# Kernel tuning notes

Hardware: AMD Instinct MI355X
Metric: run time of the kernel (lower is better)

Reference implementation:

```python
import jax, jax.numpy as jnp
import numpy as np

N = 50000   # nodes per modality sub-graph
M = 20000   # hyperedges per modality
E = 200000  # incidences per modality
D = 128     # kg_emb_dim
H = 8       # mha_n_heads
C = 64      # context entities
NE = 200000 # n_entity


def hyper_conv(x, theta, bias, node_idx, edge_idx, num_edges):
    """PyG HypergraphConv (no attention): out = D^-1 H B^-1 H^T (X Theta) + b."""
    xt = x @ theta                                   # [N, D]
    n = x.shape[0]
    ones = jnp.ones(node_idx.shape, dtype=xt.dtype)
    B = jax.ops.segment_sum(ones, edge_idx, num_segments=num_edges)   # edge degree [M]
    Dn = jax.ops.segment_sum(ones, node_idx, num_segments=n)          # node degree [N]
    Binv = jnp.where(B > 0, 1.0 / B, 0.0)
    Dinv = jnp.where(Dn > 0, 1.0 / Dn, 0.0)
    e = jax.ops.segment_sum(xt[node_idx], edge_idx, num_segments=num_edges) * Binv[:, None]
    out = jax.ops.segment_sum(e[edge_idx], node_idx, num_segments=n) * Dinv[:, None]
    return out + bias


def mha(q_in, kv, wq, bq, wk, bk, wv, bv, wo, bo, n_heads):
    """torch.nn.MultiheadAttention(batch_first) with batch=1: query=[C,D], kv=[R,D]."""
    c, d = q_in.shape
    r = kv.shape[0]
    hd = d // n_heads
    q = (q_in @ wq + bq).reshape(c, n_heads, hd).transpose(1, 0, 2)   # [H,C,hd]
    k = (kv @ wk + bk).reshape(r, n_heads, hd).transpose(1, 0, 2)     # [H,R,hd]
    v = (kv @ wv + bv).reshape(r, n_heads, hd).transpose(1, 0, 2)     # [H,R,hd]
    scores = jnp.einsum('hcd,hrd->hcr', q, k) / jnp.sqrt(jnp.asarray(hd, q.dtype))
    attn = jax.nn.softmax(scores, axis=-1)
    o = jnp.einsum('hcr,hrd->hcd', attn, v)                           # [H,C,hd]
    o = o.transpose(1, 0, 2).reshape(c, d)
    return o @ wo + bo


def setup_inputs() -> dict:
    key = jax.random.key(0)
    ks = jax.random.split(key, 24)
    s = D ** -0.5
    inp = {
        'x_item': jax.random.normal(ks[0], (N, D), jnp.float32) * s,
        'theta_item': jax.random.normal(ks[1], (D, D), jnp.float32) * s,
        'bias_item': jnp.zeros((D,), jnp.float32),
        'x_ent': jax.random.normal(ks[2], (N, D), jnp.float32) * s,
        'theta_ent': jax.random.normal(ks[3], (D, D), jnp.float32) * s,
        'bias_ent': jnp.zeros((D,), jnp.float32),
        'x_word': jax.random.normal(ks[4], (N, D), jnp.float32) * s,
        'theta_word': jax.random.normal(ks[5], (D, D), jnp.float32) * s,
        'bias_word': jnp.zeros((D,), jnp.float32),
        'context': jax.random.normal(ks[6], (C, D), jnp.float32),
        'wq': jax.random.normal(ks[7], (D, D), jnp.float32) * s,
        'bq': jnp.zeros((D,), jnp.float32),
        'wk': jax.random.normal(ks[8], (D, D), jnp.float32) * s,
        'bk': jnp.zeros((D,), jnp.float32),
        'wv': jax.random.normal(ks[9], (D, D), jnp.float32) * s,
        'bv': jnp.zeros((D,), jnp.float32),
        'wo': jax.random.normal(ks[10], (D, D), jnp.float32) * s,
        'bo': jnp.zeros((D,), jnp.float32),
        'w_rec': jax.random.normal(ks[11], (D, NE), jnp.float32) * s,
        'b_rec': jnp.zeros((NE,), jnp.float32),
        'node_item': jax.random.randint(ks[12], (E,), 0, N, jnp.int32),
        'edge_item': jax.random.randint(ks[13], (E,), 0, M, jnp.int32),
        'node_ent': jax.random.randint(ks[14], (E,), 0, N, jnp.int32),
        'edge_ent': jax.random.randint(ks[15], (E,), 0, M, jnp.int32),
        'node_word': jax.random.randint(ks[16], (E,), 0, N, jnp.int32),
        'edge_word': jax.random.randint(ks[17], (E,), 0, M, jnp.int32),
        'num_edges': M,
    }
    return inp


def reference(x_item, theta_item, bias_item, x_ent, theta_ent, bias_ent,
              x_word, theta_word, bias_word, context,
              wq, bq, wk, bk, wv, bv, wo, bo, w_rec, b_rec,
              node_item, edge_item, node_ent, edge_ent, node_word, edge_word,
              num_edges):
    # Hypergraph conv per modality (item / entity / word sub-graphs)
    item_emb = hyper_conv(x_item, theta_item, bias_item, node_item, edge_item, num_edges)
    ent_emb = hyper_conv(x_ent, theta_ent, bias_ent, node_ent, edge_ent, num_edges)
    word_emb = hyper_conv(x_word, theta_word, bias_word, node_word, edge_word, num_edges)
    # related = cat(session_embedding, knowledge_embedding) across modalities
    related = jnp.concatenate([item_emb, ent_emb, word_emb], axis=0)   # [3N, D]
    # MHItemAttention: MHA(context, related, related)
    attentive = mha(context, related, wq, bq, wk, bk, wv, bv, wo, bo, H)  # [C, D]
    # Mean pooling path of _attention_and_gating
    user_repr = jnp.mean(attentive, axis=0)                            # [D]
    user_repr = jnp.mean(jnp.concatenate([context, user_repr[None]], axis=0), axis=0)
    # rec_bias: Linear(kg_emb_dim, n_entity)
    scores = user_repr @ w_rec + b_rec                                 # [n_entity]
    return scores
```

## Files before the change

### kernel.cpp

```cpp
#include <hip/hip_runtime.h>
#include <hip/hip_bf16.h>

constexpr int N_NODES = 50000;
constexpr int M_EDGES = 20000;
constexpr int E_INC   = 200000;
constexpr int H_HEADS = 8;
constexpr int C_CTX   = 64;
constexpr int NE_OUT  = 200000;
constexpr int R_REL   = 3 * N_NODES;

constexpr int STRIPS  = 128;
constexpr int SROWS   = 1172;

constexpr int NSL   = 64;
constexpr int SE    = (M_EDGES + NSL - 1) / NSL;
constexpr int SN    = (N_NODES + NSL - 1) / NSL;
constexpr int CAP_E = 40;
constexpr int CAP_N = 24;

typedef short bf8v __attribute__((ext_vector_type(8)));
typedef float f4v  __attribute__((ext_vector_type(4)));
#define MFMA16(a, b, c) __builtin_amdgcn_mfma_f32_16x16x32_bf16(a, b, c, 0, 0, 0)

__device__ __forceinline__ unsigned short bfs(float f) {
    union { __hip_bfloat16 b; unsigned short s; } u;
    u.b = __float2bfloat16(f);
    return u.s;
}
__device__ __forceinline__ unsigned bfp(float lo, float hi) {
    union { __hip_bfloat162 b; unsigned u; } v;
    v.b = __float22bfloat162_rn(make_float2(lo, hi));
    return v.u;
}

__device__ __forceinline__ void gload16(const void* g, const void* l) {
    __builtin_amdgcn_global_load_lds(
        (const __attribute__((address_space(1))) void*)(unsigned long long)(size_t)g,
        (__attribute__((address_space(3))) void*)(unsigned)(size_t)l,
        16, 0, 0);
}

__global__ __launch_bounds__(256) void zero_kernel(float4* p, int n4) {
    int i = blockIdx.x * 256 + threadIdx.x;
    if (i < n4) p[i] = make_float4(0.f, 0.f, 0.f, 0.f);
}

__global__ __launch_bounds__(256) void wconv_kernel(
    const float* __restrict__ t0, const float* __restrict__ t1,
    const float* __restrict__ t2, unsigned short* __restrict__ out)
{
    int idx = blockIdx.x * 256 + threadIdx.x;
    int m = idx >> 14, p = idx & 16383;
    int n = p >> 7, k = p & 127;
    const float* src = (m == 0) ? t0 : (m == 1) ? t1 : t2;
    out[idx] = bfs(src[k * 128 + n]);
}

__global__ __launch_bounds__(256) void qkf_kernel(
    const float* __restrict__ ctx, const float* __restrict__ wq,
    const float* __restrict__ bq, const float* __restrict__ wk,
    const float* __restrict__ bk, unsigned short* __restrict__ qkb,
    float* __restrict__ cb)
{
    __shared__ float qrow[128];
    const int c = blockIdx.x, t = threadIdx.x;
    if (t < 128) {
        float s = bq[t];
        for (int k = 0; k < 128; ++k) s += ctx[c * 128 + k] * wq[(size_t)k * 128 + t];
        qrow[t] = s;
    }
    __syncthreads();
#pragma unroll
    for (int i = 0; i < 4; ++i) {
        int idx = t + i * 256;
        int h = idx >> 7, j = idx & 127;
        const float* wr = wk + (size_t)j * 128 + h * 16;
        const float* qr = qrow + h * 16;
        float s = 0.f;
#pragma unroll
        for (int d = 0; d < 16; ++d) s += qr[d] * wr[d];
        qkb[(size_t)(h * 64 + c) * 128 + j] = bfs(0.25f * s);
    }
    if (t < 8) {
        float s = 0.f;
#pragma unroll
        for (int d = 0; d < 16; ++d) s += qrow[t * 16 + d] * bk[t * 16 + d];
        cb[t * 64 + c] = 0.25f * s;
    }
}

__global__ __launch_bounds__(256) void xg_kernel(
    const float* __restrict__ x0, const float* __restrict__ x1,
    const float* __restrict__ x2, const unsigned short* __restrict__ thT,
    unsigned short* __restrict__ y, int R)
{
    int m = blockIdx.y;
    const float* X = (m == 0) ? x0 : (m == 1) ? x1 : x2;
    const unsigned short* W = thT + m * 16384;
    unsigned short* Y = y + (size_t)m * R * 128;
    const int w = threadIdx.x >> 6, lane = threadIdx.x & 63;
    const int ln15 = lane & 15, l16 = lane >> 4;
    const int r0 = blockIdx.x * 128 + w * 32;

    f4v acc[2][8];
#pragma unroll
    for (int i = 0; i < 2; ++i)
#pragma unroll
        for (int j = 0; j < 8; ++j) acc[i][j] = (f4v)0.f;

    for (int ks = 0; ks < 4; ++ks) {
        bf8v a[2];
#pragma unroll
        for (int mt = 0; mt < 2; ++mt) {
            int row = r0 + mt * 16 + ln15;
            row = (row < R) ? row : (R - 1);
            const float* xp = X + (size_t)row * 128 + ks * 32 + l16 * 8;
            float4 f0 = *(const float4*)xp;
            float4 f1 = *(const float4*)(xp + 4);
            union { bf8v v; unsigned w[4]; } u;
            u.w[0] = bfp(f0.x, f0.y);
            u.w[1] = bfp(f0.z, f0.w);
            u.w[2] = bfp(f1.x, f1.y);
            u.w[3] = bfp(f1.z, f1.w);
            a[mt] = u.v;
        }
#pragma unroll
        for (int nt = 0; nt < 8; ++nt) {
            bf8v b = *(const bf8v*)(W + (nt * 16 + ln15) * 128 + ks * 32 + l16 * 8);
            acc[0][nt] = MFMA16(a[0], b, acc[0][nt]);
            acc[1][nt] = MFMA16(a[1], b, acc[1][nt]);
        }
    }
#pragma unroll
    for (int mt = 0; mt < 2; ++mt)
#pragma unroll
        for (int reg = 0; reg < 4; ++reg) {
            int row = r0 + mt * 16 + l16 * 4 + reg;
            if (row < R) {
#pragma unroll
                for (int nt = 0; nt < 8; ++nt)
                    Y[(size_t)row * 128 + nt * 16 + ln15] = bfs(acc[mt][nt][reg]);
            }
        }
}

__global__ __launch_bounds__(256) void slicefill_kernel(
    const int* __restrict__ n0, const int* __restrict__ e0,
    const int* __restrict__ n1, const int* __restrict__ e1,
    const int* __restrict__ n2, const int* __restrict__ e2,
    int* __restrict__ listE, int* __restrict__ listN, int* __restrict__ cnt)
{
    const int m = blockIdx.y;
    const int* nodeA = (m == 0) ? n0 : (m == 1) ? n1 : n2;
    const int* edgeA = (m == 0) ? e0 : (m == 1) ? e1 : e2;
    int* LE = listE + (size_t)m * M_EDGES * CAP_E;
    int* LN = listN + (size_t)m * N_NODES * CAP_N;
    int* cntE = cnt + m * M_EDGES;
    int* cntN = cnt + 3 * M_EDGES + m * N_NODES;

    __shared__ int curE[SE];
    __shared__ int curN[SN];
    const int t = threadIdx.x, sl = blockIdx.x;
    const int eLo = sl * SE;
    const int eCnt = (eLo + SE <= M_EDGES) ? SE : (M_EDGES - eLo);
    const int nLo = sl * SN;
    const int nCnt = (nLo + SN <= N_NODES) ? SN : (N_NODES - nLo);

    for (int j = t; j < SE; j += 256) curE[j] = 0;
    for (int j = t; j < SN; j += 256) curN[j] = 0;
    __syncthreads();

    const int4* e4 = (const int4*)edgeA;
    const int4* n4 = (const int4*)nodeA;
    for (int ii = t * 2; ii < E_INC / 4; ii += 512) {
        int4 ea = e4[ii], na = n4[ii];
        int4 eb = e4[ii + 1], nb = n4[ii + 1];
        int ev[8] = {ea.x, ea.y, ea.z, ea.w, eb.x, eb.y, eb.z, eb.w};
        int nv[8] = {na.x, na.y, na.z, na.w, nb.x, nb.y, nb.z, nb.w};
#pragma unroll
        for (int k = 0; k < 8; ++k) {
            int e = ev[k], n = nv[k];
            if ((unsigned)(e - eLo) < (unsigned)eCnt) {
                int s = atomicAdd(&curE[e - eLo], 1);
                if (s < CAP_E) LE[(size_t)e * CAP_E + s] = n;
            }
            if ((unsigned)(n - nLo) < (unsigned)nCnt) {
                int s = atomicAdd(&curN[n - nLo], 1);
                if (s < CAP_N) LN[(size_t)n * CAP_N + s] = e;
            }
        }
    }
    __syncthreads();
    for (int j = t; j < eCnt; j += 256) cntE[eLo + j] = curE[j];
    for (int j = t; j < nCnt; j += 256) cntN[nLo + j] = curN[j];
}

#define ACC8(v) do { \
    a0 += __uint_as_float((v).x << 16); a1 += __uint_as_float((v).x & 0xFFFF0000u); \
    a2 += __uint_as_float((v).y << 16); a3 += __uint_as_float((v).y & 0xFFFF0000u); \
    a4 += __uint_as_float((v).z << 16); a5 += __uint_as_float((v).z & 0xFFFF0000u); \
    a6 += __uint_as_float((v).w << 16); a7 += __uint_as_float((v).w & 0xFFFF0000u); } while (0)

__global__ __launch_bounds__(256) void gedge_kernel(
    const unsigned short* __restrict__ xt,
    const int* __restrict__ listE, const int* __restrict__ cnt,
    unsigned short* __restrict__ eb)
{
    int mm = blockIdx.y;
    const unsigned short* X = xt + (size_t)mm * N_NODES * 128;
    unsigned short* Eo = eb + (size_t)mm * M_EDGES * 128;
    int t = blockIdx.x * 256 + threadIdx.x;
    int e = t >> 4, lane = t & 15;
    if (e >= M_EDGES) return;
    const int* seg = listE + ((size_t)mm * M_EDGES + e) * CAP_E;
    int en = cnt[mm * M_EDGES + e];
    float a0 = 0, a1 = 0, a2 = 0, a3 = 0, a4 = 0, a5 = 0, a6 = 0, a7 = 0;
    int j = 0;
    for (; j + 4 <= en; j += 4) {
        int n0 = seg[j], n1 = seg[j + 1], n2 = seg[j + 2], n3 = seg[j + 3];
        uint4 v0 = *(const uint4*)(X + (size_t)n0 * 128 + lane * 8);
        uint4 v1 = *(const uint4*)(X + (size_t)n1 * 128 + lane * 8);
        uint4 v2 = *(const uint4*)(X + (size_t)n2 * 128 + lane * 8);
        uint4 v3 = *(const uint4*)(X + (size_t)n3 * 128 + lane * 8);
        ACC8(v0); ACC8(v1); ACC8(v2); ACC8(v3);
    }
    for (; j < en; ++j) {
        int n = seg[j];
        uint4 v = *(const uint4*)(X + (size_t)n * 128 + lane * 8);
        ACC8(v);
    }
    float bi = (en > 0) ? 1.f / (float)en : 0.f;
    uint4 o;
    o.x = bfp(a0 * bi, a1 * bi);
    o.y = bfp(a2 * bi, a3 * bi);
    o.z = bfp(a4 * bi, a5 * bi);
    o.w = bfp(a6 * bi, a7 * bi);
    *(uint4*)(Eo + (size_t)e * 128 + lane * 8) = o;
}

__global__ __launch_bounds__(256) void gnode_kernel(
    const unsigned short* __restrict__ eb,
    const int* __restrict__ listN, const int* __restrict__ cnt,
    const float* __restrict__ b0, const float* __restrict__ b1,
    const float* __restrict__ b2, unsigned short* __restrict__ rel)
{
    int mm = blockIdx.y;
    const unsigned short* E = eb + (size_t)mm * M_EDGES * 128;
    const float* bias = (mm == 0) ? b0 : (mm == 1) ? b1 : b2;
    unsigned short* R = rel + (size_t)mm * N_NODES * 128;
    int t = blockIdx.x * 256 + threadIdx.x;
    int n = t >> 4, lane = t & 15;
    if (n >= N_NODES) return;
    const int* seg = listN + ((size_t)mm * N_NODES + n) * CAP_N;
    int en = cnt[3 * M_EDGES + mm * N_NODES + n];
    float a0 = 0, a1 = 0, a2 = 0, a3 = 0, a4 = 0, a5 = 0, a6 = 0, a7 = 0;
    int j = 0;
    for (; j + 4 <= en; j += 4) {
        int e0 = seg[j], e1 = seg[j + 1], e2 = seg[j + 2], e3 = seg[j + 3];
        uint4 v0 = *(const uint4*)(E + (size_t)e0 * 128 + lane * 8);
        uint4 v1 = *(const uint4*)(E + (size_t)e1 * 128 + lane * 8);
        uint4 v2 = *(const uint4*)(E + (size_t)e2 * 128 + lane * 8);
        uint4 v3 = *(const uint4*)(E + (size_t)e3 * 128 + lane * 8);
        ACC8(v0); ACC8(v1); ACC8(v2); ACC8(v3);
    }
    for (; j < en; ++j) {
        int e = seg[j];
        uint4 v = *(const uint4*)(E + (size_t)e * 128 + lane * 8);
        ACC8(v);
    }
    float di = (en > 0) ? 1.f / (float)en : 0.f;
    uint4 o;
    o.x = bfp(a0 * di + bias[lane * 8 + 0], a1 * di + bias[lane * 8 + 1]);
    o.y = bfp(a2 * di + bias[lane * 8 + 2], a3 * di + bias[lane * 8 + 3]);
    o.z = bfp(a4 * di + bias[lane * 8 + 4], a5 * di + bias[lane * 8 + 5]);
    o.w = bfp(a6 * di + bias[lane * 8 + 6], a7 * di + bias[lane * 8 + 7]);
    *(uint4*)(R + (size_t)n * 128 + lane * 8) = o;
}

__global__ __launch_bounds__(256) void attn_kernel(
    const unsigned short* __restrict__ rel, const unsigned short* __restrict__ qkb,
    const float* __restrict__ cb, float* __restrict__ PRpart, float* __restrict__ lpart)
{
    __shared__ __align__(16) unsigned char relN[2][16384];
    __shared__ __align__(16) unsigned char relTb[16384];
    __shared__ __align__(16) unsigned char Plb[16384];

    const int strip = blockIdx.x, pair = blockIdx.y;
    const int t = threadIdx.x, w = t >> 6, lane = t & 63;
    const int ln15 = lane & 15, l16 = lane >> 4;
    const int aswz = (ln15 & 7) << 4;

    bf8v bq[2][4];
#pragma unroll
    for (int nt = 0; nt < 2; ++nt)
#pragma unroll
        for (int ks = 0; ks < 4; ++ks)
            bq[nt][ks] = *(const bf8v*)(qkb +
                (size_t)(pair * 128 + w * 32 + nt * 16 + ln15) * 128 + ks * 32 + l16 * 8);
    float cbr[2];
#pragma unroll
    for (int nt = 0; nt < 2; ++nt)
        cbr[nt] = cb[pair * 128 + w * 32 + nt * 16 + ln15];

    f4v pr[2][8];
#pragma unroll
    for (int i = 0; i < 2; ++i)
#pragma unroll
        for (int j = 0; j < 8; ++j) pr[i][j] = (f4v)0.f;
    float lacc[2] = {0.f, 0.f};

    const int r0s = strip * SROWS;
    const int rend = (r0s + SROWS < R_REL) ? (r0s + SROWS) : R_REL;
    const int nchunk = (rend - r0s + 63) >> 6;

    auto stage = [&](int base, int b) {
#pragma unroll
        for (int k = 0; k < 4; ++k) {
            int o = k * 4096 + w * 1024 + lane * 16;
            int rr = o >> 8;
            int cbyte = (o & 255) ^ ((rr & 7) << 4);
            gload16(rel + (size_t)(base + rr) * 128 + (cbyte >> 1),
                    &relN[b][k * 4096 + w * 1024]);
        }
    };

    stage(r0s, 0);
    int cur = 0;
    for (int c = 0; c < nchunk; ++c) {
        const int base = r0s + c * 64;
        const int nvalid = rend - base;

        if (c + 1 < nchunk) {
            stage(base + 64, cur ^ 1);
            __builtin_amdgcn_sched_barrier(0);
            asm volatile("s_waitcnt vmcnt(4)" ::: "memory");
        } else {
            __builtin_amdgcn_sched_barrier(0);
            asm volatile("s_waitcnt vmcnt(0)" ::: "memory");
        }
        __builtin_amdgcn_sched_barrier(0);
        __builtin_amdgcn_s_barrier();
        __builtin_amdgcn_sched_barrier(0);

        const unsigned char* RN = relN[cur];

#pragma unroll
        for (int a2 = 0; a2 < 2; ++a2) {
            int idx = t + a2 * 256;
            int rp = idx & 31, jg = idx >> 5;
            int r2 = rp * 2;
            uint4 A = *(const uint4*)(RN + r2 * 256 + ((jg * 16) ^ ((r2 & 7) << 4)));
            uint4 B = *(const uint4*)(RN + (r2 + 1) * 256 + ((jg * 16) ^ (((r2 + 1) & 7) << 4)));
            unsigned aw[4] = {A.x, A.y, A.z, A.w};
            unsigned bw[4] = {B.x, B.y, B.z, B.w};
#pragma unroll
            for (int jj = 0; jj < 4; ++jj) {
                int j0 = jg * 8 + jj * 2;
                *(unsigned*)(relTb + j0 * 128 + ((rp * 4) ^ ((jj * 2) << 4))) =
                    (aw[jj] & 0xFFFFu) | (bw[jj] << 16);
                *(unsigned*)(relTb + (j0 + 1) * 128 + ((rp * 4) ^ ((jj * 2 + 1) << 4))) =
                    (aw[jj] >> 16) | (bw[jj] & 0xFFFF0000u);
            }
        }

        f4v sc[4][2];
#pragma unroll
        for (int i = 0; i < 4; ++i) { sc[i][0] = (f4v)0.f; sc[i][1] = (f4v)0.f; }
        __builtin_amdgcn_s_setprio(1);
#pragma unroll
        for (int ks = 0; ks < 4; ++ks) {
            bf8v a[4];
#pragma unroll
            for (int mt = 0; mt < 4; ++mt)
                a[mt] = *(const bf8v*)(RN + (mt * 16 + ln15) * 256 +
                                       ((ks * 64 + l16 * 16) ^ aswz));
#pragma unroll
            for (int mt = 0; mt < 4; ++mt) {
                sc[mt][0] = MFMA16(a[mt], bq[0][ks], sc[mt][0]);
                sc[mt][1] = MFMA16(a[mt], bq[1][ks], sc[mt][1]);
            }
        }
        __builtin_amdgcn_s_setprio(0);

        bool full = (nvalid >= 64);
#pragma unroll
        for (int nt = 0; nt < 2; ++nt) {
            float ls = 0.f;
#pragma unroll
            for (int mt = 0; mt < 4; ++mt) {
                float pv[4];
#pragma unroll
                for (int reg = 0; reg < 4; ++reg) {
                    int rl = mt * 16 + l16 * 4 + reg;
                    float p = __expf(sc[mt][nt][reg] + cbr[nt]);
                    if (!full && rl >= nvalid) p = 0.f;
                    ls += p;
                    pv[reg] = p;
                }
                int hc = w * 32 + nt * 16 + ln15;
                int pb = hc * 128 + ((mt * 32 + l16 * 8) ^ aswz);
                *(uint2*)(Plb + pb) = make_uint2(bfp(pv[0], pv[1]), bfp(pv[2], pv[3]));
            }
            ls += __shfl_xor(ls, 16, 64);
            ls += __shfl_xor(ls, 32, 64);
            lacc[nt] += ls;
        }

        asm volatile("s_waitcnt lgkmcnt(0)" ::: "memory");
        __builtin_amdgcn_sched_barrier(0);
        __builtin_amdgcn_s_barrier();
        __builtin_amdgcn_sched_barrier(0);

        __builtin_amdgcn_s_setprio(1);
#pragma unroll
        for (int ks = 0; ks < 2; ++ks) {
            bf8v ap[2];
#pragma unroll
            for (int mt = 0; mt < 2; ++mt) {
                int hc = w * 32 + mt * 16 + ln15;
                ap[mt] = *(const bf8v*)(Plb + hc * 128 + ((ks * 64 + l16 * 16) ^ aswz));
            }
#pragma unroll
            for (int nt = 0; nt < 8; ++nt) {
                int j = nt * 16 + ln15;
                bf8v b = *(const bf8v*)(relTb + j * 128 + ((ks * 64 + l16 * 16) ^ aswz));
                pr[0][nt] = MFMA16(ap[0], b, pr[0][nt]);
                pr[1][nt] = MFMA16(ap[1], b, pr[1][nt]);
            }
        }
        __builtin_amdgcn_s_setprio(0);
        cur ^= 1;
    }

    float* PB = PRpart + (size_t)(pair * STRIPS + strip) * 128 * 128;
#pragma unroll
    for (int mt = 0; mt < 2; ++mt)
#pragma unroll
        for (int reg = 0; reg < 4; ++reg) {
            int hcl = w * 32 + mt * 16 + l16 * 4 + reg;
#pragma unroll
            for (int nt = 0; nt < 8; ++nt)
                PB[hcl * 128 + nt * 16 + ln15] = pr[mt][nt][reg];
        }
    if (lane < 16) {
        float* LB = lpart + (size_t)(pair * STRIPS + strip) * 128;
        LB[w * 32 + ln15] = lacc[0];
        LB[w * 32 + 16 + ln15] = lacc[1];
    }
}

__global__ __launch_bounds__(256) void reduce_kernel(
    const float* __restrict__ PRpart, const float* __restrict__ lpart,
    const float* __restrict__ wv, const float* __restrict__ bv,
    float* __restrict__ osum)
{
    int hc = blockIdx.x;
    int pair = hc >> 7, hcl = hc & 127, h = hc >> 6;
    __shared__ float PS[128];
    __shared__ float LL[129];
    int t = threadIdx.x;
    if (t < 128) {
        float s = 0.f;
        const float* p = PRpart + ((size_t)(pair * STRIPS) * 128 + hcl) * 128 + t;
        for (int st = 0; st < STRIPS; ++st) s += p[(size_t)st * 128 * 128];
        PS[t] = s;
    } else {
        int idx = t - 128;
        LL[idx] = lpart[(size_t)(pair * STRIPS + idx) * 128 + hcl];
    }
    __syncthreads();
    if (t == 0) {
        float l = 0.f;
        for (int st = 0; st < 128; ++st) l += LL[st];
        LL[128] = l;
    }
    __syncthreads();
    if (t < 16) {
        float o = 0.f;
        for (int j = 0; j < 128; ++j) o += PS[j] * wv[(size_t)j * 128 + h * 16 + t];
        float on = o / LL[128] + bv[h * 16 + t];
        atomicAdd(&osum[h * 16 + t], on);
    }
}

__global__ __launch_bounds__(128) void user_kernel(
    const float* __restrict__ ctx, const float* __restrict__ osum,
    const float* __restrict__ wo, const float* __restrict__ bo,
    float* __restrict__ u)
{
    __shared__ float os[128];
    int d = threadIdx.x;
    os[d] = osum[d];
    __syncthreads();
    float cs = 0.f;
    for (int cc = 0; cc < 64; ++cc) cs += ctx[cc * 128 + d];
    float ow = 0.f;
    for (int j = 0; j < 128; ++j) ow += os[j] * wo[j * 128 + d];
    u[d] = (cs + ow * (1.f / 64.f) + bo[d]) * (1.f / 65.f);
}

__global__ __launch_bounds__(256) void rec_kernel(
    const float* __restrict__ u, const float* __restrict__ wrec,
    const float* __restrict__ brec, float* __restrict__ out)
{
    __shared__ float ul[128];
    if (threadIdx.x < 128) ul[threadIdx.x] = u[threadIdx.x];
    __syncthreads();
    int j = blockIdx.x * 256 + threadIdx.x;
    if (j >= NE_OUT) return;
    float a0 = brec[j], a1 = 0.f, a2 = 0.f, a3 = 0.f;
#pragma unroll 4
    for (int d = 0; d < 128; d += 4) {
        a0 += ul[d + 0] * wrec[(size_t)(d + 0) * NE_OUT + j];
        a1 += ul[d + 1] * wrec[(size_t)(d + 1) * NE_OUT + j];
        a2 += ul[d + 2] * wrec[(size_t)(d + 2) * NE_OUT + j];
        a3 += ul[d + 3] * wrec[(size_t)(d + 3) * NE_OUT + j];
    }
    out[j] = (a0 + a1) + (a2 + a3);
}

extern "C" void kernel_launch(void* const* d_in, const int* in_sizes, int n_in,
                              void* d_out, int out_size, void* d_ws, size_t ws_size,
                              hipStream_t stream)
{
    const float* ctx  = (const float*)d_in[9];
    const float* wq = (const float*)d_in[10];
    const float* bq = (const float*)d_in[11];
    const float* wk = (const float*)d_in[12];
    const float* bk = (const float*)d_in[13];
    const float* wv = (const float*)d_in[14];
    const float* bv = (const float*)d_in[15];
    const float* wo = (const float*)d_in[16];
    const float* bo = (const float*)d_in[17];
    const float* wrec = (const float*)d_in[18];
    const float* brec = (const float*)d_in[19];
    const int* node0 = (const int*)d_in[20];
    const int* edge0 = (const int*)d_in[21];
    const int* node1 = (const int*)d_in[22];
    const int* edge1 = (const int*)d_in[23];
    const int* node2 = (const int*)d_in[24];
    const int* edge2 = (const int*)d_in[25];
    float* out = (float*)d_out;

    char* ws = (char*)d_ws;
    size_t off = 0;
    auto alloc = [&](size_t nbytes) {
        void* p = ws + off;
        off += (nbytes + 255) & ~(size_t)255;
        return p;
    };
    unsigned short* rel  = (unsigned short*)alloc((size_t)R_REL * 128 * 2);
    unsigned short* xt   = (unsigned short*)alloc((size_t)3 * N_NODES * 128 * 2);
    unsigned short* eb   = (unsigned short*)alloc((size_t)3 * M_EDGES * 128 * 2);
    float* PRpart = (float*)alloc((size_t)4 * STRIPS * 128 * 128 * 4);
    float* lpart  = (float*)alloc((size_t)4 * STRIPS * 128 * 4);
    unsigned short* qkb = (unsigned short*)alloc(512 * 128 * 2);
    float* cbv    = (float*)alloc(512 * 4);
    unsigned short* thT = (unsigned short*)alloc(3 * 16384 * 2);
    int* cnt      = (int*)alloc((size_t)(3 * M_EDGES + 3 * N_NODES) * 4);
    float* osum   = (float*)alloc(128 * 4);
    int* listE    = (int*)alloc((size_t)3 * M_EDGES * CAP_E * 4);
    int* listN    = (int*)alloc((size_t)3 * N_NODES * CAP_N * 4);
    float* u      = (float*)alloc(128 * 4);
    (void)ws_size; (void)in_sizes; (void)n_in; (void)out_size;

    zero_kernel<<<1, 256, 0, stream>>>((float4*)osum, 32);
    slicefill_kernel<<<dim3(NSL, 3), 256, 0, stream>>>(
        node0, edge0, node1, edge1, node2, edge2, listE, listN, cnt);
    wconv_kernel<<<192, 256, 0, stream>>>((const float*)d_in[1], (const float*)d_in[4],
                                          (const float*)d_in[7], thT);
    qkf_kernel<<<64, 256, 0, stream>>>(ctx, wq, bq, wk, bk, qkb, cbv);
    xg_kernel<<<dim3((N_NODES + 127) / 128, 3), 256, 0, stream>>>(
        (const float*)d_in[0], (const float*)d_in[3], (const float*)d_in[6], thT, xt, N_NODES);
    gedge_kernel<<<dim3(M_EDGES * 16 / 256, 3), 256, 0, stream>>>(xt, listE, cnt, eb);
    gnode_kernel<<<dim3(N_NODES * 16 / 256, 3), 256, 0, stream>>>(
        eb, listN, cnt, (const float*)d_in[2], (const float*)d_in[5],
        (const float*)d_in[8], rel);
    attn_kernel<<<dim3(STRIPS, 4), 256, 0, stream>>>(rel, qkb, cbv, PRpart, lpart);
    reduce_kernel<<<512, 256, 0, stream>>>(PRpart, lpart, wv, bv, osum);
    user_kernel<<<1, 128, 0, stream>>>(ctx, osum, wo, bo, u);
    rec_kernel<<<(NE_OUT + 255) / 256, 256, 0, stream>>>(u, wrec, brec, out);
}
```

Before: 571.4 us.

## Replace sliced shared-memory bucketing with global-atomic incidence list fill

The previous fill kernel had each of 64 slices per modality scan all incidences and keep only the ones in its range, using shared-memory counters. The new kernel gives each thread four incidences and claims list slots with global atomics on the count arrays. The count arrays (and osum, now packed next to them) are zeroed by a wider zero kernel. The redundant full scans are gone, at the cost of global atomic contention and a nondeterministic order within each list. The degree used for normalization is now the true count, while the gathers are capped at the list capacity.

```diff
diff --git a/kernel.cpp b/kernel.cpp
--- a/kernel.cpp
+++ b/kernel.cpp
@@ -12,9 +12,6 @@
 constexpr int STRIPS  = 128;
 constexpr int SROWS   = 1172;
 
-constexpr int NSL   = 64;
-constexpr int SE    = (M_EDGES + NSL - 1) / NSL;
-constexpr int SN    = (N_NODES + NSL - 1) / NSL;
 constexpr int CAP_E = 40;
 constexpr int CAP_N = 24;
 
@@ -144,7 +141,7 @@
         }
 }
 
-__global__ __launch_bounds__(256) void slicefill_kernel(
+__global__ __launch_bounds__(256) void fillx_kernel(
     const int* __restrict__ n0, const int* __restrict__ e0,
     const int* __restrict__ n1, const int* __restrict__ e1,
     const int* __restrict__ n2, const int* __restrict__ e2,
@@ -158,41 +155,23 @@
     int* cntE = cnt + m * M_EDGES;
     int* cntN = cnt + 3 * M_EDGES + m * N_NODES;
 
-    __shared__ int curE[SE];
-    __shared__ int curN[SN];
-    const int t = threadIdx.x, sl = blockIdx.x;
-    const int eLo = sl * SE;
-    const int eCnt = (eLo + SE <= M_EDGES) ? SE : (M_EDGES - eLo);
-    const int nLo = sl * SN;
-    const int nCnt = (nLo + SN <= N_NODES) ? SN : (N_NODES - nLo);
-
-    for (int j = t; j < SE; j += 256) curE[j] = 0;
-    for (int j = t; j < SN; j += 256) curN[j] = 0;
-    __syncthreads();
-
-    const int4* e4 = (const int4*)edgeA;
-    const int4* n4 = (const int4*)nodeA;
-    for (int ii = t * 2; ii < E_INC / 4; ii += 512) {
-        int4 ea = e4[ii], na = n4[ii];
-        int4 eb = e4[ii + 1], nb = n4[ii + 1];
-        int ev[8] = {ea.x, ea.y, ea.z, ea.w, eb.x, eb.y, eb.z, eb.w};
-        int nv[8] = {na.x, na.y, na.z, na.w, nb.x, nb.y, nb.z, nb.w};
-#pragma unroll
-        for (int k = 0; k < 8; ++k) {
-            int e = ev[k], n = nv[k];
-            if ((unsigned)(e - eLo) < (unsigned)eCnt) {
-                int s = atomicAdd(&curE[e - eLo], 1);
-                if (s < CAP_E) LE[(size_t)e * CAP_E + s] = n;
-            }
-            if ((unsigned)(n - nLo) < (unsigned)nCnt) {
-                int s = atomicAdd(&curN[n - nLo], 1);
-                if (s < CAP_N) LN[(size_t)n * CAP_N + s] = e;
-            }
-        }
-    }
-    __syncthreads();
-    for (int j = t; j < eCnt; j += 256) cntE[eLo + j] = curE[j];
-    for (int j = t; j < nCnt; j += 256) cntN[nLo + j] = curN[j];
+    int i0 = (blockIdx.x * 256 + threadIdx.x) * 4;
+    if (i0 >= E_INC) return;
+    int4 ev = *(const int4*)(edgeA + i0);
+    int4 nv = *(const int4*)(nodeA + i0);
+    int e[4] = {ev.x, ev.y, ev.z, ev.w};
+    int n[4] = {nv.x, nv.y, nv.z, nv.w};
+    int se[4], sn[4];
+#pragma unroll
+    for (int k = 0; k < 4; ++k) se[k] = atomicAdd(&cntE[e[k]], 1);
+#pragma unroll
+    for (int k = 0; k < 4; ++k) sn[k] = atomicAdd(&cntN[n[k]], 1);
+#pragma unroll
+    for (int k = 0; k < 4; ++k)
+        if (se[k] < CAP_E) LE[(size_t)e[k] * CAP_E + se[k]] = n[k];
+#pragma unroll
+    for (int k = 0; k < 4; ++k)
+        if (sn[k] < CAP_N) LN[(size_t)n[k] * CAP_N + sn[k]] = e[k];
 }
 
 #define ACC8(v) do { \
@@ -213,7 +192,8 @@
     int e = t >> 4, lane = t & 15;
     if (e >= M_EDGES) return;
     const int* seg = listE + ((size_t)mm * M_EDGES + e) * CAP_E;
-    int en = cnt[mm * M_EDGES + e];
+    int deg = cnt[mm * M_EDGES + e];
+    int en = (deg < CAP_E) ? deg : CAP_E;
     float a0 = 0, a1 = 0, a2 = 0, a3 = 0, a4 = 0, a5 = 0, a6 = 0, a7 = 0;
     int j = 0;
     for (; j + 4 <= en; j += 4) {
@@ -229,7 +209,7 @@
         uint4 v = *(const uint4*)(X + (size_t)n * 128 + lane * 8);
         ACC8(v);
     }
-    float bi = (en > 0) ? 1.f / (float)en : 0.f;
+    float bi = (deg > 0) ? 1.f / (float)deg : 0.f;
     uint4 o;
     o.x = bfp(a0 * bi, a1 * bi);
     o.y = bfp(a2 * bi, a3 * bi);
@@ -252,7 +232,8 @@
     int n = t >> 4, lane = t & 15;
     if (n >= N_NODES) return;
     const int* seg = listN + ((size_t)mm * N_NODES + n) * CAP_N;
-    int en = cnt[3 * M_EDGES + mm * N_NODES + n];
+    int deg = cnt[3 * M_EDGES + mm * N_NODES + n];
+    int en = (deg < CAP_N) ? deg : CAP_N;
     float a0 = 0, a1 = 0, a2 = 0, a3 = 0, a4 = 0, a5 = 0, a6 = 0, a7 = 0;
     int j = 0;
     for (; j + 4 <= en; j += 4) {
@@ -268,7 +249,7 @@
         uint4 v = *(const uint4*)(E + (size_t)e * 128 + lane * 8);
         ACC8(v);
     }
-    float di = (en > 0) ? 1.f / (float)en : 0.f;
+    float di = (deg > 0) ? 1.f / (float)deg : 0.f;
     uint4 o;
     o.x = bfp(a0 * di + bias[lane * 8 + 0], a1 * di + bias[lane * 8 + 1]);
     o.y = bfp(a2 * di + bias[lane * 8 + 2], a3 * di + bias[lane * 8 + 3]);
@@ -557,15 +538,18 @@
     unsigned short* qkb = (unsigned short*)alloc(512 * 128 * 2);
     float* cbv    = (float*)alloc(512 * 4);
     unsigned short* thT = (unsigned short*)alloc(3 * 16384 * 2);
-    int* cnt      = (int*)alloc((size_t)(3 * M_EDGES + 3 * N_NODES) * 4);
-    float* osum   = (float*)alloc(128 * 4);
+    int* cnt      = (int*)alloc((size_t)(3 * M_EDGES + 3 * N_NODES + 128) * 4);
+    float* osum   = (float*)(cnt + 3 * M_EDGES + 3 * N_NODES);
     int* listE    = (int*)alloc((size_t)3 * M_EDGES * CAP_E * 4);
     int* listN    = (int*)alloc((size_t)3 * N_NODES * CAP_N * 4);
     float* u      = (float*)alloc(128 * 4);
     (void)ws_size; (void)in_sizes; (void)n_in; (void)out_size;
 
-    zero_kernel<<<1, 256, 0, stream>>>((float4*)osum, 32);
-    slicefill_kernel<<<dim3(NSL, 3), 256, 0, stream>>>(
+    {
+        int nwords = 3 * M_EDGES + 3 * N_NODES + 128;
+        zero_kernel<<<(nwords / 4 + 255) / 256, 256, 0, stream>>>((float4*)cnt, nwords / 4);
+    }
+    fillx_kernel<<<dim3((E_INC / 4 + 255) / 256, 3), 256, 0, stream>>>(
         node0, edge0, node1, edge1, node2, edge2, listE, listN, cnt);
     wconv_kernel<<<192, 256, 0, stream>>>((const float*)d_in[1], (const float*)d_in[4],
                                           (const float*)d_in[7], thT);
```

New measurement: 503.1 us. 1.14x faster.
